# Kernel tuning notes

Hardware: AMD Instinct MI355X
Metric: run time of the kernel (lower is better)

Reference implementation:

```python
import jax, jax.numpy as jnp
import numpy as np

B, N, C_IN, H, C_OUT = 8, 1024, 256, 4, 256
C = C_OUT // H  # per-head dim = 64
ALPHA = 0.2
NEG_INF = -9e15


def setup_inputs() -> dict:
    key = jax.random.key(0)
    k1, k2, k3, k4, k5 = jax.random.split(key, 5)
    node_feats = jax.random.normal(k1, (B, N, C_IN), dtype=jnp.float32)
    adj_matrix = jax.random.randint(k2, (B, N, N), 0, 2, dtype=jnp.int32)
    # include self-loops as GAT expects
    eye = jnp.eye(N, dtype=jnp.int32)[None]
    adj_matrix = jnp.maximum(adj_matrix, eye)
    # xavier_uniform with gain=1.414
    def xavier(k, shape, fan_in, fan_out, gain=1.414):
        lim = gain * np.sqrt(6.0 / (fan_in + fan_out))
        return jax.random.uniform(k, shape, jnp.float32, -lim, lim)
    W = xavier(k3, (C_OUT, C_IN), C_IN, C_OUT)          # projection weight [out,in]
    b = jnp.zeros((C_OUT,), dtype=jnp.float32)           # projection bias
    a = xavier(k4, (H, 2 * C), 2 * C, H)                 # attention vector per head
    return {"node_feats": node_feats, "adj_matrix": adj_matrix, "W": W, "b": b, "a": a}


def reference(node_feats, adj_matrix, W, b, a):
    Bb, Nn, _ = node_feats.shape
    Hh, twoC = a.shape
    Cc = twoC // 2
    # linear projection -> [B, N, H, C]
    h = (node_feats @ W.T + b).reshape(Bb, Nn, Hh, Cc)
    # edge logit(i,j) = leakyrelu(a . [h_i, h_j]) = leakyrelu(a1.h_i + a2.h_j)
    a_src, a_dst = a[:, :Cc], a[:, Cc:]
    l_src = jnp.einsum('bihc,hc->bih', h, a_src)  # [B,N,H]
    l_dst = jnp.einsum('bjhc,hc->bjh', h, a_dst)  # [B,N,H]
    logits = jax.nn.leaky_relu(l_src[:, :, None, :] + l_dst[:, None, :, :], ALPHA)  # [B,N,N,H]
    logits = jnp.where(adj_matrix[..., None] == 1, logits, NEG_INF)
    probs = jax.nn.softmax(logits, axis=2)  # softmax over neighbors j
    out = jnp.einsum('bijh,bjhc->bihc', probs, h)  # aggregate
    return out.reshape(Bb, Nn, Hh * Cc)  # concat heads
```

## Files before the change

### kernel.cpp

```cpp
#include <hip/hip_runtime.h>
#include <hip/hip_bf16.h>

#define BN   8
#define NN   1024
#define CIN  256
#define COUT 256
#define HH   4
#define CC   64
#define ALPHA_C 0.2f

typedef __attribute__((ext_vector_type(8))) short short8;
typedef __attribute__((ext_vector_type(4))) float f32x4;

__device__ __forceinline__ unsigned short f2bf(float x) {
    __hip_bfloat16 h = __float2bfloat16(x);
    return *(unsigned short*)&h;
}
__device__ __forceinline__ float bf2f(unsigned short u) {
    return __uint_as_float(((unsigned int)u) << 16);
}

__global__ __launch_bounds__(256) void k0_wpack(
    const float* __restrict__ W, unsigned short* __restrict__ Whp, unsigned short* __restrict__ Wlp)
{
    const int bid = blockIdx.x;
    const int n = threadIdx.x;
    const int fi = n * 64 + (bid >> 2) * 8 + (bid & 3) * 2;
    const float4* W4 = (const float4*)W;
    float4 wa = W4[fi], wb = W4[fi + 1];
    float xs[8] = {wa.x, wa.y, wa.z, wa.w, wb.x, wb.y, wb.z, wb.w};
    unsigned short hh[8], ll[8];
    #pragma unroll
    for (int e = 0; e < 8; ++e) {
        hh[e] = f2bf(xs[e]);
        ll[e] = f2bf(xs[e] - bf2f(hh[e]));
    }
    *(uint4*)(Whp + ((size_t)bid * 256 + n) * 8) = *(uint4*)hh;
    *(uint4*)(Wlp + ((size_t)bid * 256 + n) * 8) = *(uint4*)ll;
}

__global__ __launch_bounds__(1024, 1) void k1_gemm(
    const float* __restrict__ X, const float* __restrict__ bias, const float* __restrict__ a,
    const unsigned short* __restrict__ Whp, const unsigned short* __restrict__ Wlp,
    unsigned short* __restrict__ hbf_p, float* __restrict__ lsrc_t, float* __restrict__ ldst_t)
{
    __shared__ __align__(16) unsigned short Xh[32 * 256];
    __shared__ __align__(16) unsigned short Xl[32 * 256];
    __shared__ float lsP[2][8][2][16];

    const int bid = blockIdx.x;
    const int row0 = bid * 32;
    const int b  = bid >> 5;
    const int tj = bid & 31;
    const int tid = threadIdx.x;
    const int wv = tid >> 6, l = tid & 63, il = l & 15, jg = l >> 4;
    const int mq = wv >> 3, no = wv & 7;

    {
        const float4* X4 = (const float4*)(X + (size_t)row0 * CIN);
        #pragma unroll
        for (int it = 0; it < 2; ++it) {
            int f = it * 1024 + tid;
            int r = f >> 6, k4 = f & 63;
            float4 x = X4[f];
            unsigned short h0 = f2bf(x.x), h1 = f2bf(x.y), h2 = f2bf(x.z), h3 = f2bf(x.w);
            unsigned short l0 = f2bf(x.x - bf2f(h0)), l1 = f2bf(x.y - bf2f(h1));
            unsigned short l2 = f2bf(x.z - bf2f(h2)), l3 = f2bf(x.w - bf2f(h3));
            unsigned short hs[4] = {h0, h1, h2, h3}, ls[4] = {l0, l1, l2, l3};
            int off = r * 512 + ((k4 * 8) ^ ((r & 7) << 4));
            *(uint2*)((char*)Xh + off) = *(uint2*)hs;
            *(uint2*)((char*)Xl + off) = *(uint2*)ls;
        }
    }
    __syncthreads();

    f32x4 acc0 = {0.f, 0.f, 0.f, 0.f}, acc1 = acc0;
    {
        const int abase = (mq * 16 + il) * 512;
        const int swz = (il & 7) << 4;
        const short8* Wh8 = (const short8*)Whp;
        const short8* Wl8 = (const short8*)Wlp;
        const int nb = no * 32 + il;
        #pragma unroll
        for (int kc = 0; kc < 8; ++kc) {
            const int ab = abase + ((kc * 64 + jg * 16) ^ swz);
            short8 Ah = *(const short8*)((const char*)Xh + ab);
            short8 Al = *(const short8*)((const char*)Xl + ab);
            const int pidx = (kc * 4 + jg) * 256 + nb;
            short8 Bh0 = Wh8[pidx],      Bl0 = Wl8[pidx];
            short8 Bh1 = Wh8[pidx + 16], Bl1 = Wl8[pidx + 16];
            acc0 = __builtin_amdgcn_mfma_f32_16x16x32_bf16(Ah, Bh0, acc0, 0, 0, 0);
            acc1 = __builtin_amdgcn_mfma_f32_16x16x32_bf16(Ah, Bh1, acc1, 0, 0, 0);
            acc0 = __builtin_amdgcn_mfma_f32_16x16x32_bf16(Ah, Bl0, acc0, 0, 0, 0);
            acc1 = __builtin_amdgcn_mfma_f32_16x16x32_bf16(Ah, Bl1, acc1, 0, 0, 0);
            acc0 = __builtin_amdgcn_mfma_f32_16x16x32_bf16(Al, Bh0, acc0, 0, 0, 0);
            acc1 = __builtin_amdgcn_mfma_f32_16x16x32_bf16(Al, Bh1, acc1, 0, 0, 0);
        }
    }

    const int c0 = no * 32 + il, c1 = c0 + 16;
    const float bia0 = bias[c0], bia1 = bias[c1];
    const int hh = no >> 1;
    const int cc0 = c0 & 63, cc1 = c1 & 63;
    const float as0 = a[hh * 128 + cc0],      as1 = a[hh * 128 + cc1];
    const float ad0 = a[hh * 128 + 64 + cc0], ad1 = a[hh * 128 + 64 + cc1];

    float v0[4], v1[4], psrc[4], pdst[4];
    #pragma unroll
    for (int r = 0; r < 4; ++r) {
        v0[r] = acc0[r] + bia0;
        v1[r] = acc1[r] + bia1;
        psrc[r] = v0[r] * as0 + v1[r] * as1;
        pdst[r] = v0[r] * ad0 + v1[r] * ad1;
    }
    #pragma unroll
    for (int off = 8; off >= 1; off >>= 1) {
        #pragma unroll
        for (int r = 0; r < 4; ++r) {
            psrc[r] += __shfl_xor(psrc[r], off);
            pdst[r] += __shfl_xor(pdst[r], off);
        }
    }
    __syncthreads();

    unsigned short* hp = Xh;
    #pragma unroll
    for (int r = 0; r < 4; ++r) {
        int m = mq * 16 + 4 * jg + r;
        int base = (m >> 3) * 128 + (m & 7);
        hp[(c0 >> 6) * 2048 + ((c0 & 63) >> 4) * 512 + base + (c0 & 15) * 8] = f2bf(v0[r]);
        hp[(c1 >> 6) * 2048 + ((c1 & 63) >> 4) * 512 + base + (c1 & 15) * 8] = f2bf(v1[r]);
    }
    if (il == 0) {
        #pragma unroll
        for (int r = 0; r < 4; ++r) {
            lsP[0][no][mq][4 * jg + r] = psrc[r];
            lsP[1][no][mq][4 * jg + r] = pdst[r];
        }
    }
    __syncthreads();

    {
        uint4* dst4 = (uint4*)(hbf_p + (size_t)(b * 32 + tj) * 8192);
        dst4[tid] = ((const uint4*)hp)[tid];
    }
    if (tid < 256) {
        int sd = tid >> 7, rem = tid & 127, h2 = rem >> 5, m = rem & 31;
        float v = lsP[sd][2 * h2][m >> 4][m & 15] + lsP[sd][2 * h2 + 1][m >> 4][m & 15];
        float* dst = sd ? ldst_t : lsrc_t;
        dst[((size_t)b * HH + h2) * NN + tj * 32 + m] = v;
    }
}

__global__ __launch_bounds__(1024, 2) void k2_attn(
    const unsigned short* __restrict__ hbf_p, const int* __restrict__ adj,
    const float* __restrict__ lsrc_t, const float* __restrict__ ldst_t,
    float* __restrict__ out)
{
    __shared__ __align__(16) char smem[32768];
    __shared__ float lsumS[4][4][16];

    unsigned int (*adjw)[16] = (unsigned int (*)[16])smem;
    float* ldsTbl = (float*)(smem + 2048);

    const int bid = blockIdx.x;
    const int b  = bid & 7;
    const int i0 = (bid >> 3) * 16;
    const int tid = threadIdx.x;
    const int wv = tid >> 6, l = tid & 63, il = l & 15, jg = l >> 4;
    const int h = wv & 3, jh = wv >> 2;

    {
        const int* arow = adj + ((size_t)b * NN + i0 + wv) * NN;
        #pragma unroll
        for (int it = 0; it < 16; ++it) {
            int av = arow[it * 64 + l];
            unsigned long long mb = __ballot(av != 0);
            if (l == 0) {
                adjw[2 * it    ][wv] = (unsigned int)mb;
                adjw[2 * it + 1][wv] = (unsigned int)(mb >> 32);
            }
        }
    }
    ((float4*)ldsTbl)[tid] = ((const float4*)(ldst_t + (size_t)b * HH * NN))[tid];
    const float lsrc_v = lsrc_t[((size_t)b * HH + h) * NN + i0 + il];

    __syncthreads();

    float mx = -3.4e38f;
    #pragma unroll
    for (int jt = 0; jt < 16; ++jt) mx = fmaxf(mx, ldsTbl[h * 1024 + jt * 64 + l]);
    #pragma unroll
    for (int off = 32; off >= 1; off >>= 1) mx = fmaxf(mx, __shfl_xor(mx, off));
    const float t0  = lsrc_v + mx;
    const float m_r = fmaxf(t0, ALPHA_C * t0);
    float lsum = 0.f;

    f32x4 acc0 = {0.f,0.f,0.f,0.f}, acc1 = acc0, acc2 = acc0, acc3 = acc0;

    const short8* bfp = (const short8*)(hbf_p + (size_t)b * 32 * 8192);
    const int fb = h * 256 + l;
    const float* ltb = ldsTbl + h * 1024 + jg * 8;

    #pragma unroll 2
    for (int t = 0; t < 8; ++t) {
        const int tj = jh * 8 + t;
        short8 c0 = bfp[tj * 1024 + fb +   0];
        short8 c1 = bfp[tj * 1024 + fb +  64];
        short8 c2 = bfp[tj * 1024 + fb + 128];
        short8 c3 = bfp[tj * 1024 + fb + 192];
        const unsigned int bw = adjw[tj][il] >> (jg * 8);
        const float4 dA = *(const float4*)(ltb + tj * 32);
        const float4 dB = *(const float4*)(ltb + tj * 32 + 4);

        short8 af;
        #define PELEM(DV, E) {                                   \
            float s_ = lsrc_v + (DV);                            \
            s_ = fmaxf(s_, ALPHA_C * s_);                        \
            float p_ = __expf(s_ - m_r);                         \
            p_ = ((bw >> (E)) & 1u) ? p_ : 0.f;                  \
            lsum += p_;                                          \
            af[E] = (short)f2bf(p_); }
        PELEM(dA.x, 0) PELEM(dA.y, 1) PELEM(dA.z, 2) PELEM(dA.w, 3)
        PELEM(dB.x, 4) PELEM(dB.y, 5) PELEM(dB.z, 6) PELEM(dB.w, 7)
        #undef PELEM

        acc0 = __builtin_amdgcn_mfma_f32_16x16x32_bf16(af, c0, acc0, 0, 0, 0);
        acc1 = __builtin_amdgcn_mfma_f32_16x16x32_bf16(af, c1, acc1, 0, 0, 0);
        acc2 = __builtin_amdgcn_mfma_f32_16x16x32_bf16(af, c2, acc2, 0, 0, 0);
        acc3 = __builtin_amdgcn_mfma_f32_16x16x32_bf16(af, c3, acc3, 0, 0, 0);
    }

    lsum += __shfl_xor(lsum, 16);
    lsum += __shfl_xor(lsum, 32);
    if (l < 16) lsumS[jh][h][il] = lsum;
    __syncthreads();

    float* red = (float*)smem;
    float* rb = red + (jh & 1) * 4096;
    #define STOREALL(OP) {                                                    \
        const int base = (4 * jg) * 256 + h * 64 + il;                        \
        rb[base +   0 +  0] OP acc0[0]; rb[base +   0 + 16] OP acc1[0];       \
        rb[base +   0 + 32] OP acc2[0]; rb[base +   0 + 48] OP acc3[0];       \
        rb[base + 256 +  0] OP acc0[1]; rb[base + 256 + 16] OP acc1[1];       \
        rb[base + 256 + 32] OP acc2[1]; rb[base + 256 + 48] OP acc3[1];       \
        rb[base + 512 +  0] OP acc0[2]; rb[base + 512 + 16] OP acc1[2];       \
        rb[base + 512 + 32] OP acc2[2]; rb[base + 512 + 48] OP acc3[2];       \
        rb[base + 768 +  0] OP acc0[3]; rb[base + 768 + 16] OP acc1[3];       \
        rb[base + 768 + 32] OP acc2[3]; rb[base + 768 + 48] OP acc3[3]; }
    if (jh < 2) STOREALL(=)
    __syncthreads();
    if (jh >= 2) STOREALL(+=)
    __syncthreads();
    #undef STOREALL

    #pragma unroll
    for (int e = 0; e < 4; ++e) {
        int flat = e * 1024 + tid;
        int m = flat >> 8, c = flat & 255;
        int h2 = c >> 6;
        float v  = red[flat] + red[4096 + flat];
        float ls = lsumS[0][h2][m] + lsumS[1][h2][m] + lsumS[2][h2][m] + lsumS[3][h2][m];
        out[((size_t)(b * NN + i0 + m)) * COUT + c] = v / ls;
    }
}

extern "C" void kernel_launch(void* const* d_in, const int* in_sizes, int n_in,
                              void* d_out, int out_size, void* d_ws, size_t ws_size,
                              hipStream_t stream) {
    const float* X    = (const float*)d_in[0];
    const int*   adj  = (const int*)  d_in[1];
    const float* W    = (const float*)d_in[2];
    const float* bias = (const float*)d_in[3];
    const float* a    = (const float*)d_in[4];
    float* out = (float*)d_out;

    unsigned short* hbf_p = (unsigned short*)d_ws;
    float* lsrc_t = (float*)(hbf_p + (size_t)BN * 32 * 8192);
    float* ldst_t = lsrc_t + (size_t)BN * HH * NN;
    unsigned short* Whp = (unsigned short*)(ldst_t + (size_t)BN * HH * NN);
    unsigned short* Wlp = Whp + 65536;

    k0_wpack<<<32, 256, 0, stream>>>(W, Whp, Wlp);
    k1_gemm<<<256, 1024, 0, stream>>>(X, bias, a, Whp, Wlp, hbf_p, lsrc_t, ldst_t);
    k2_attn<<<BN * (NN / 16), 1024, 0, stream>>>(hbf_p, adj, lsrc_t, ldst_t, out);
}
```

Baseline: 49.72 us.

## Pre-pack adjacency to bitmask and retile attention to 64 rows × 2 heads

Adds a separate kernel that compresses the int32 adjacency matrix into a global bitmask. The attention kernel now processes 64 query rows and 2 heads per block instead of 16 rows and all heads, giving 256 blocks. Each loaded bf16 h fragment is reused across four row groups, which cuts redundant global loads of h. In exchange there is an extra launch, more accumulator registers, larger LDS use (about 66KB) and a multi-pass reduction with more barriers.

```diff
diff --git a/kernel.cpp b/kernel.cpp
--- a/kernel.cpp
+++ b/kernel.cpp
@@ -37,6 +37,24 @@
     }
     *(uint4*)(Whp + ((size_t)bid * 256 + n) * 8) = *(uint4*)hh;
     *(uint4*)(Wlp + ((size_t)bid * 256 + n) * 8) = *(uint4*)ll;
+}
+
+__global__ __launch_bounds__(256) void ka_adjpack(
+    const int* __restrict__ adj, unsigned int* __restrict__ bmG)
+{
+    const int wv = threadIdx.x >> 6;
+    const int l  = threadIdx.x & 63;
+    const int row = blockIdx.x * 4 + wv;
+    const int* arow = adj + (size_t)row * NN;
+    #pragma unroll 4
+    for (int it = 0; it < 16; ++it) {
+        int av = arow[it * 64 + l];
+        unsigned long long mb = __ballot(av != 0);
+        if (l == 0) {
+            bmG[row * 32 + 2 * it    ] = (unsigned int)mb;
+            bmG[row * 32 + 2 * it + 1] = (unsigned int)(mb >> 32);
+        }
+    }
 }
 
 __global__ __launch_bounds__(1024, 1) void k1_gemm(
@@ -153,115 +171,166 @@
 }
 
 __global__ __launch_bounds__(1024, 2) void k2_attn(
-    const unsigned short* __restrict__ hbf_p, const int* __restrict__ adj,
+    const unsigned short* __restrict__ hbf_p, const unsigned int* __restrict__ bmG,
     const float* __restrict__ lsrc_t, const float* __restrict__ ldst_t,
     float* __restrict__ out)
 {
-    __shared__ __align__(16) char smem[32768];
-    __shared__ float lsumS[4][4][16];
-
-    unsigned int (*adjw)[16] = (unsigned int (*)[16])smem;
-    float* ldsTbl = (float*)(smem + 2048);
+    __shared__ __align__(16) char smem[66048];
+    __shared__ float lsumS[8][2][64];
+
+    unsigned int* bmLDS = (unsigned int*)smem;
+    float* ldsTbl = (float*)(smem + 8448);
 
     const int bid = blockIdx.x;
     const int b  = bid & 7;
-    const int i0 = (bid >> 3) * 16;
+    const int it = (bid >> 3) & 15;
+    const int hp = bid >> 7;
+    const int i0 = it * 64;
     const int tid = threadIdx.x;
     const int wv = tid >> 6, l = tid & 63, il = l & 15, jg = l >> 4;
-    const int h = wv & 3, jh = wv >> 2;
-
-    {
-        const int* arow = adj + ((size_t)b * NN + i0 + wv) * NN;
-        #pragma unroll
-        for (int it = 0; it < 16; ++it) {
-            int av = arow[it * 64 + l];
-            unsigned long long mb = __ballot(av != 0);
-            if (l == 0) {
-                adjw[2 * it    ][wv] = (unsigned int)mb;
-                adjw[2 * it + 1][wv] = (unsigned int)(mb >> 32);
-            }
-        }
-    }
-    ((float4*)ldsTbl)[tid] = ((const float4*)(ldst_t + (size_t)b * HH * NN))[tid];
-    const float lsrc_v = lsrc_t[((size_t)b * HH + h) * NN + i0 + il];
+    const int h2 = wv & 1, jq8 = wv >> 1;
+    const int h = hp * 2 + h2;
+
+    {
+        const unsigned int* src = bmG + ((size_t)(b * NN + i0)) * 32;
+        #pragma unroll
+        for (int k = 0; k < 2; ++k) {
+            int idx = k * 1024 + tid;
+            bmLDS[(idx >> 5) * 33 + (idx & 31)] = src[idx];
+        }
+        const float2* ls2 = (const float2*)(ldst_t + ((size_t)(b * HH + hp * 2)) * NN);
+        ((float2*)ldsTbl)[tid] = ls2[tid];
+    }
+    const float* lsrc_b = lsrc_t + ((size_t)(b * HH + h)) * NN + i0;
+    const float lsv0 = lsrc_b[il];
+    const float lsv1 = lsrc_b[16 + il];
+    const float lsv2 = lsrc_b[32 + il];
+    const float lsv3 = lsrc_b[48 + il];
 
     __syncthreads();
 
     float mx = -3.4e38f;
     #pragma unroll
-    for (int jt = 0; jt < 16; ++jt) mx = fmaxf(mx, ldsTbl[h * 1024 + jt * 64 + l]);
+    for (int jt = 0; jt < 16; ++jt) mx = fmaxf(mx, ldsTbl[h2 * 1024 + jt * 64 + l]);
     #pragma unroll
     for (int off = 32; off >= 1; off >>= 1) mx = fmaxf(mx, __shfl_xor(mx, off));
-    const float t0  = lsrc_v + mx;
-    const float m_r = fmaxf(t0, ALPHA_C * t0);
-    float lsum = 0.f;
-
-    f32x4 acc0 = {0.f,0.f,0.f,0.f}, acc1 = acc0, acc2 = acc0, acc3 = acc0;
+    float mr0, mr1, mr2, mr3;
+    { float t_ = lsv0 + mx; mr0 = fmaxf(t_, ALPHA_C * t_); }
+    { float t_ = lsv1 + mx; mr1 = fmaxf(t_, ALPHA_C * t_); }
+    { float t_ = lsv2 + mx; mr2 = fmaxf(t_, ALPHA_C * t_); }
+    { float t_ = lsv3 + mx; mr3 = fmaxf(t_, ALPHA_C * t_); }
+    float ls0 = 0.f, ls1 = 0.f, ls2 = 0.f, ls3 = 0.f;
+
+    f32x4 z4 = {0.f,0.f,0.f,0.f};
+    f32x4 a00 = z4, a01 = z4, a02 = z4, a03 = z4;
+    f32x4 a10 = z4, a11 = z4, a12 = z4, a13 = z4;
+    f32x4 a20 = z4, a21 = z4, a22 = z4, a23 = z4;
+    f32x4 a30 = z4, a31 = z4, a32 = z4, a33 = z4;
 
     const short8* bfp = (const short8*)(hbf_p + (size_t)b * 32 * 8192);
-    const int fb = h * 256 + l;
-    const float* ltb = ldsTbl + h * 1024 + jg * 8;
-
-    #pragma unroll 2
-    for (int t = 0; t < 8; ++t) {
-        const int tj = jh * 8 + t;
-        short8 c0 = bfp[tj * 1024 + fb +   0];
-        short8 c1 = bfp[tj * 1024 + fb +  64];
-        short8 c2 = bfp[tj * 1024 + fb + 128];
-        short8 c3 = bfp[tj * 1024 + fb + 192];
-        const unsigned int bw = adjw[tj][il] >> (jg * 8);
+    const int fbase = h * 256 + l;
+    const float* ltb = ldsTbl + h2 * 1024 + jg * 8;
+
+    #define PEL(AF, E, DV, BWV, LSV, MR, LS) {               \
+        float s_ = (LSV) + (DV);                             \
+        s_ = fmaxf(s_, ALPHA_C * s_);                        \
+        float p_ = __expf(s_ - (MR));                        \
+        p_ = ((BWV >> (E)) & 1u) ? p_ : 0.f;                 \
+        LS += p_;                                            \
+        AF[E] = (short)f2bf(p_); }
+
+    #define ROWG(G, C0, C1, C2, C3) {                        \
+        const unsigned int bwv = bw##G >> (jg * 8);          \
+        short8 af;                                           \
+        PEL(af, 0, dA.x, bwv, lsv##G, mr##G, ls##G)          \
+        PEL(af, 1, dA.y, bwv, lsv##G, mr##G, ls##G)          \
+        PEL(af, 2, dA.z, bwv, lsv##G, mr##G, ls##G)          \
+        PEL(af, 3, dA.w, bwv, lsv##G, mr##G, ls##G)          \
+        PEL(af, 4, dB.x, bwv, lsv##G, mr##G, ls##G)          \
+        PEL(af, 5, dB.y, bwv, lsv##G, mr##G, ls##G)          \
+        PEL(af, 6, dB.z, bwv, lsv##G, mr##G, ls##G)          \
+        PEL(af, 7, dB.w, bwv, lsv##G, mr##G, ls##G)          \
+        C0 = __builtin_amdgcn_mfma_f32_16x16x32_bf16(af, c0, C0, 0, 0, 0); \
+        C1 = __builtin_amdgcn_mfma_f32_16x16x32_bf16(af, c1, C1, 0, 0, 0); \
+        C2 = __builtin_amdgcn_mfma_f32_16x16x32_bf16(af, c2, C2, 0, 0, 0); \
+        C3 = __builtin_amdgcn_mfma_f32_16x16x32_bf16(af, c3, C3, 0, 0, 0); }
+
+    #pragma unroll
+    for (int t = 0; t < 4; ++t) {
+        const int tj = jq8 * 4 + t;
+        short8 c0 = bfp[tj * 1024 + fbase +   0];
+        short8 c1 = bfp[tj * 1024 + fbase +  64];
+        short8 c2 = bfp[tj * 1024 + fbase + 128];
+        short8 c3 = bfp[tj * 1024 + fbase + 192];
+        const unsigned int bw0 = bmLDS[( 0 + il) * 33 + tj];
+        const unsigned int bw1 = bmLDS[(16 + il) * 33 + tj];
+        const unsigned int bw2 = bmLDS[(32 + il) * 33 + tj];
+        const unsigned int bw3 = bmLDS[(48 + il) * 33 + tj];
         const float4 dA = *(const float4*)(ltb + tj * 32);
         const float4 dB = *(const float4*)(ltb + tj * 32 + 4);
 
-        short8 af;
-        #define PELEM(DV, E) {                                   \
-            float s_ = lsrc_v + (DV);                            \
-            s_ = fmaxf(s_, ALPHA_C * s_);                        \
-            float p_ = __expf(s_ - m_r);                         \
-            p_ = ((bw >> (E)) & 1u) ? p_ : 0.f;                  \
-            lsum += p_;                                          \
-            af[E] = (short)f2bf(p_); }
-        PELEM(dA.x, 0) PELEM(dA.y, 1) PELEM(dA.z, 2) PELEM(dA.w, 3)
-        PELEM(dB.x, 4) PELEM(dB.y, 5) PELEM(dB.z, 6) PELEM(dB.w, 7)
-        #undef PELEM
-
-        acc0 = __builtin_amdgcn_mfma_f32_16x16x32_bf16(af, c0, acc0, 0, 0, 0);
-        acc1 = __builtin_amdgcn_mfma_f32_16x16x32_bf16(af, c1, acc1, 0, 0, 0);
-        acc2 = __builtin_amdgcn_mfma_f32_16x16x32_bf16(af, c2, acc2, 0, 0, 0);
-        acc3 = __builtin_amdgcn_mfma_f32_16x16x32_bf16(af, c3, acc3, 0, 0, 0);
-    }
-
-    lsum += __shfl_xor(lsum, 16);
-    lsum += __shfl_xor(lsum, 32);
-    if (l < 16) lsumS[jh][h][il] = lsum;
-    __syncthreads();
-
-    float* red = (float*)smem;
-    float* rb = red + (jh & 1) * 4096;
-    #define STOREALL(OP) {                                                    \
-        const int base = (4 * jg) * 256 + h * 64 + il;                        \
-        rb[base +   0 +  0] OP acc0[0]; rb[base +   0 + 16] OP acc1[0];       \
-        rb[base +   0 + 32] OP acc2[0]; rb[base +   0 + 48] OP acc3[0];       \
-        rb[base + 256 +  0] OP acc0[1]; rb[base + 256 + 16] OP acc1[1];       \
-        rb[base + 256 + 32] OP acc2[1]; rb[base + 256 + 48] OP acc3[1];       \
-        rb[base + 512 +  0] OP acc0[2]; rb[base + 512 + 16] OP acc1[2];       \
-        rb[base + 512 + 32] OP acc2[2]; rb[base + 512 + 48] OP acc3[2];       \
-        rb[base + 768 +  0] OP acc0[3]; rb[base + 768 + 16] OP acc1[3];       \
-        rb[base + 768 + 32] OP acc2[3]; rb[base + 768 + 48] OP acc3[3]; }
-    if (jh < 2) STOREALL(=)
-    __syncthreads();
-    if (jh >= 2) STOREALL(+=)
-    __syncthreads();
-    #undef STOREALL
-
-    #pragma unroll
-    for (int e = 0; e < 4; ++e) {
+        ROWG(0, a00, a01, a02, a03)
+        ROWG(1, a10, a11, a12, a13)
+        ROWG(2, a20, a21, a22, a23)
+        ROWG(3, a30, a31, a32, a33)
+    }
+    #undef PEL
+    #undef ROWG
+
+    ls0 += __shfl_xor(ls0, 16); ls0 += __shfl_xor(ls0, 32);
+    ls1 += __shfl_xor(ls1, 16); ls1 += __shfl_xor(ls1, 32);
+    ls2 += __shfl_xor(ls2, 16); ls2 += __shfl_xor(ls2, 32);
+    ls3 += __shfl_xor(ls3, 16); ls3 += __shfl_xor(ls3, 32);
+    if (l < 16) {
+        lsumS[jq8][h2][ 0 + il] = ls0;
+        lsumS[jq8][h2][16 + il] = ls1;
+        lsumS[jq8][h2][32 + il] = ls2;
+        lsumS[jq8][h2][48 + il] = ls3;
+    }
+    __syncthreads();
+
+    float* red0 = (float*)smem;
+    float* red1 = red0 + 64 * 129;
+    {
+        float* rb = (jq8 & 1) ? red1 : red0;
+        const int cb = h2 * 64 + il;
+        #define STROW(ACC, RG, CS, OP) {                                     \
+            rb[(RG * 16 + 4 * jg + 0) * 129 + cb + CS * 16] OP ACC[0];       \
+            rb[(RG * 16 + 4 * jg + 1) * 129 + cb + CS * 16] OP ACC[1];       \
+            rb[(RG * 16 + 4 * jg + 2) * 129 + cb + CS * 16] OP ACC[2];       \
+            rb[(RG * 16 + 4 * jg + 3) * 129 + cb + CS * 16] OP ACC[3]; }
+        #define STOREALL(OP) {                                               \
+            STROW(a00, 0, 0, OP) STROW(a01, 0, 1, OP)                        \
+            STROW(a02, 0, 2, OP) STROW(a03, 0, 3, OP)                        \
+            STROW(a10, 1, 0, OP) STROW(a11, 1, 1, OP)                        \
+            STROW(a12, 1, 2, OP) STROW(a13, 1, 3, OP)                        \
+            STROW(a20, 2, 0, OP) STROW(a21, 2, 1, OP)                        \
+            STROW(a22, 2, 2, OP) STROW(a23, 2, 3, OP)                        \
+            STROW(a30, 3, 0, OP) STROW(a31, 3, 1, OP)                        \
+            STROW(a32, 3, 2, OP) STROW(a33, 3, 3, OP) }
+        if (jq8 < 2) STOREALL(=)
+        __syncthreads();
+        if (jq8 >= 2 && jq8 < 4) STOREALL(+=)
+        __syncthreads();
+        if (jq8 >= 4 && jq8 < 6) STOREALL(+=)
+        __syncthreads();
+        if (jq8 >= 6) STOREALL(+=)
+        __syncthreads();
+        #undef STROW
+        #undef STOREALL
+    }
+
+    #pragma unroll
+    for (int e = 0; e < 8; ++e) {
         int flat = e * 1024 + tid;
-        int m = flat >> 8, c = flat & 255;
-        int h2 = c >> 6;
-        float v  = red[flat] + red[4096 + flat];
-        float ls = lsumS[0][h2][m] + lsumS[1][h2][m] + lsumS[2][h2][m] + lsumS[3][h2][m];
-        out[((size_t)(b * NN + i0 + m)) * COUT + c] = v / ls;
+        int row = flat >> 7, c = flat & 127;
+        int h2o = c >> 6;
+        float v  = red0[row * 129 + c] + red1[row * 129 + c];
+        float ls = lsumS[0][h2o][row] + lsumS[1][h2o][row]
+                 + lsumS[2][h2o][row] + lsumS[3][h2o][row]
+                 + lsumS[4][h2o][row] + lsumS[5][h2o][row]
+                 + lsumS[6][h2o][row] + lsumS[7][h2o][row];
+        out[((size_t)(b * NN + i0 + row)) * COUT + hp * 128 + c] = v / ls;
     }
 }
 
@@ -280,8 +349,10 @@
     float* ldst_t = lsrc_t + (size_t)BN * HH * NN;
     unsigned short* Whp = (unsigned short*)(ldst_t + (size_t)BN * HH * NN);
     unsigned short* Wlp = Whp + 65536;
+    unsigned int*   bmG = (unsigned int*)(Wlp + 65536);
 
     k0_wpack<<<32, 256, 0, stream>>>(W, Whp, Wlp);
+    ka_adjpack<<<(BN * NN) / 4, 256, 0, stream>>>(adj, bmG);
     k1_gemm<<<256, 1024, 0, stream>>>(X, bias, a, Whp, Wlp, hbf_p, lsrc_t, ldst_t);
-    k2_attn<<<BN * (NN / 16), 1024, 0, stream>>>(hbf_p, adj, lsrc_t, ldst_t, out);
-}
+    k2_attn<<<256, 1024, 0, stream>>>(hbf_p, bmG, lsrc_t, ldst_t, out);
+}
```

New measurement: 51.25 us. 1.03x slower.

## Pre-pack adjacency into bitmask in separate kernel before attention

Applied to the files above, without the earlier changes.

Moves the int32 adjacency-to-bitmask ballot packing out of the attention kernel into a dedicated kernel launched before the GEMM, writing a compact bitmask to workspace. The attention kernel then loads only 2 KB of bitmask per block instead of 64 KB of int32 adjacency, shortening its prologue. It also remaps the GEMM block index to interleave batches. This adds an extra launch and a 32 MB adjacency read in its own kernel, which may not overlap with other work since everything runs on one stream.

```diff
diff --git a/kernel.cpp b/kernel.cpp
--- a/kernel.cpp
+++ b/kernel.cpp
@@ -39,6 +39,27 @@
     *(uint4*)(Wlp + ((size_t)bid * 256 + n) * 8) = *(uint4*)ll;
 }
 
+__global__ __launch_bounds__(256) void ka_adjpack(
+    const int* __restrict__ adj, unsigned int* __restrict__ bmG)
+{
+    const int bid = blockIdx.x;
+    const int b  = bid & 7;
+    const int rl = bid >> 3;
+    const int wv = threadIdx.x >> 6;
+    const int l  = threadIdx.x & 63;
+    const int row = b * NN + rl * 4 + wv;
+    const int* arow = adj + (size_t)row * NN;
+    #pragma unroll 4
+    for (int it = 0; it < 16; ++it) {
+        int av = arow[it * 64 + l];
+        unsigned long long mb = __ballot(av != 0);
+        if (l == 0) {
+            bmG[row * 32 + 2 * it    ] = (unsigned int)mb;
+            bmG[row * 32 + 2 * it + 1] = (unsigned int)(mb >> 32);
+        }
+    }
+}
+
 __global__ __launch_bounds__(1024, 1) void k1_gemm(
     const float* __restrict__ X, const float* __restrict__ bias, const float* __restrict__ a,
     const unsigned short* __restrict__ Whp, const unsigned short* __restrict__ Wlp,
@@ -49,9 +70,9 @@
     __shared__ float lsP[2][8][2][16];
 
     const int bid = blockIdx.x;
-    const int row0 = bid * 32;
-    const int b  = bid >> 5;
-    const int tj = bid & 31;
+    const int b  = bid & 7;
+    const int tj = bid >> 3;
+    const int row0 = b * NN + tj * 32;
     const int tid = threadIdx.x;
     const int wv = tid >> 6, l = tid & 63, il = l & 15, jg = l >> 4;
     const int mq = wv >> 3, no = wv & 7;
@@ -153,7 +174,7 @@
 }
 
 __global__ __launch_bounds__(1024, 2) void k2_attn(
-    const unsigned short* __restrict__ hbf_p, const int* __restrict__ adj,
+    const unsigned short* __restrict__ hbf_p, const unsigned int* __restrict__ bmG,
     const float* __restrict__ lsrc_t, const float* __restrict__ ldst_t,
     float* __restrict__ out)
 {
@@ -170,17 +191,10 @@
     const int wv = tid >> 6, l = tid & 63, il = l & 15, jg = l >> 4;
     const int h = wv & 3, jh = wv >> 2;
 
-    {
-        const int* arow = adj + ((size_t)b * NN + i0 + wv) * NN;
-        #pragma unroll
-        for (int it = 0; it < 16; ++it) {
-            int av = arow[it * 64 + l];
-            unsigned long long mb = __ballot(av != 0);
-            if (l == 0) {
-                adjw[2 * it    ][wv] = (unsigned int)mb;
-                adjw[2 * it + 1][wv] = (unsigned int)(mb >> 32);
-            }
-        }
+    if (tid < 512) {
+        const unsigned int* src = bmG + ((size_t)(b * NN + i0)) * 32;
+        int row = tid >> 5, jw = tid & 31;
+        adjw[jw][row] = src[row * 32 + jw];
     }
     ((float4*)ldsTbl)[tid] = ((const float4*)(ldst_t + (size_t)b * HH * NN))[tid];
     const float lsrc_v = lsrc_t[((size_t)b * HH + h) * NN + i0 + il];
@@ -280,8 +294,10 @@
     float* ldst_t = lsrc_t + (size_t)BN * HH * NN;
     unsigned short* Whp = (unsigned short*)(ldst_t + (size_t)BN * HH * NN);
     unsigned short* Wlp = Whp + 65536;
+    unsigned int*   bmG = (unsigned int*)(Wlp + 65536);
 
     k0_wpack<<<32, 256, 0, stream>>>(W, Whp, Wlp);
+    ka_adjpack<<<(BN * NN) / 4, 256, 0, stream>>>(adj, bmG);
     k1_gemm<<<256, 1024, 0, stream>>>(X, bias, a, Whp, Wlp, hbf_p, lsrc_t, ldst_t);
-    k2_attn<<<BN * (NN / 16), 1024, 0, stream>>>(hbf_p, adj, lsrc_t, ldst_t, out);
-}
+    k2_attn<<<BN * (NN / 16), 1024, 0, stream>>>(hbf_p, bmG, lsrc_t, ldst_t, out);
+}
```

Measured after the change: 46.94 us. 1.06x faster.
